# Kernel tuning notes

Measured on AMD Instinct MI355X. Metric: run time of the kernel, lower is better.

The kernel has to match this reference:

```python
import jax, jax.numpy as jnp
import numpy as np

DATA_NUM = 1024
CLS_NUM = 32000


def setup_inputs() -> dict:
    key = jax.random.key(0)
    k1, k2, k3, k4 = jax.random.split(key, 4)
    h1 = jax.random.normal(k1, (DATA_NUM, 2), dtype=jnp.float32) + 3.0
    e1 = jax.random.normal(k2, (CLS_NUM, 2), dtype=jnp.float32)
    h3 = jax.random.normal(k3, (DATA_NUM, 2), dtype=jnp.float32) * 2.0
    e3 = jax.random.normal(k4, (CLS_NUM, 2), dtype=jnp.float32)
    return {"h1": h1, "e1": e1, "h3": h3, "e3": e3, "share_head": 0}


def cal_akl(l1, l2):
    # l1: student logits (D, C); l2: teacher logits (D, C)
    probs1 = jax.nn.softmax(l1, axis=-1)
    probs2 = jax.nn.softmax(l2, axis=-1)
    # sort teacher probs ascending; gather student probs in same order
    sorted_idx = jnp.argsort(probs2, axis=-1)
    sorted_probs2 = jnp.take_along_axis(probs2, sorted_idx, axis=-1)
    sorted_probs1 = jnp.take_along_axis(probs1, sorted_idx, axis=-1)
    gap = jnp.abs(sorted_probs2 - sorted_probs1)
    cum_probs2 = jnp.cumsum(sorted_probs2, axis=-1)
    tail_mask = (cum_probs2 < 0.5).astype(l1.dtype)
    g_head = jax.lax.stop_gradient(jnp.sum(gap * (1.0 - tail_mask), axis=-1))
    g_tail = jax.lax.stop_gradient(jnp.sum(gap * tail_mask, axis=-1))
    lprobs1 = jax.nn.log_softmax(l1, axis=-1)
    lprobs2 = jax.nn.log_softmax(l2, axis=-1)
    fkl = jnp.sum(probs2 * (lprobs2 - lprobs1), axis=-1)
    rkl = jnp.sum(probs1 * (lprobs1 - lprobs2), axis=-1)
    denom = g_head + g_tail
    akl = (g_head / denom) * fkl + (g_tail / denom) * rkl
    return jnp.mean(akl)


def reference(h1, e1, h3, e3, share_head):
    # share_head is a static Python int/bool; obj == 'akl', share_head == 0 path
    if share_head:
        raise NotImplementedError("reference covers share_head=False path")
    stu_logits = h1 @ e1.T   # (D, C)
    tea_logits = h3 @ e3.T   # (D, C)
    return cal_akl(stu_logits, tea_logits)
```

## Files before the change

### kernel.cpp

```cpp
#include <hip/hip_runtime.h>
#include <math.h>

#define DNUM 1024
#define CNUM 32000
#define NT 512
#define R 2
#define GRID (DNUM / R)
#define KC 4
#define KF 8
#define NQ (CNUM / 4)
#define NFULL (NQ / NT)
#define TAILN (NQ - NFULL*NT)

#define L2E 1.4426950408889634f
#define LN2 0.6931471805599453f

typedef float v2f __attribute__((ext_vector_type(2)));

__device__ __forceinline__ v2f splat2(float s) { v2f v; v.x = s; v.y = s; return v; }

__device__ __forceinline__ float wave_red_sum(float v) {
    #pragma unroll
    for (int o = 32; o > 0; o >>= 1) v += __shfl_down(v, o, 64);
    return v;
}

__global__ __launch_bounds__(NT, 4) void akl_rows(
    const float* __restrict__ h1, const float* __restrict__ e1,
    const float* __restrict__ h3, const float* __restrict__ e3,
    float* __restrict__ out)
{
    const int tid  = threadIdx.x;
    const int lane = tid & 63, wid = tid >> 6;
    const int row0 = blockIdx.x * R;

    __shared__ float pool[16384];
    __shared__ float red[48];
    __shared__ float shCS[R*KC];
    __shared__ float shFP[R*KF], shFG[R*KF];
    __shared__ float shA[R][7];

    float a1L[R], b1L[R], a2L[R], b2L[R], mh1L[R], mh2L[R], icwC[R], c0C[R];
    #pragma unroll
    for (int r = 0; r < R; r++) {
        a1L[r] = h1[2*(row0+r)] * L2E; b1L[r] = h1[2*(row0+r)+1] * L2E;
        a2L[r] = h3[2*(row0+r)] * L2E; b2L[r] = h3[2*(row0+r)+1] * L2E;
        mh1L[r] = 6.0f * (fabsf(a1L[r]) + fabsf(b1L[r]));
        mh2L[r] = 6.0f * (fabsf(a2L[r]) + fabsf(b2L[r]));
        float sp = fmaxf(sqrtf(a2L[r]*a2L[r] + b2L[r]*b2L[r]), 1e-6f);
        icwC[r] = 1.0f / (1.35f * sp);
        c0C[r] = 0.5f/1.35f + mh2L[r]*icwC[r];
    }
    for (int i = tid; i < 16384; i += NT) pool[i] = 0.f;
    __syncthreads();

    const float4* __restrict__ E1 = (const float4*)e1;
    const float4* __restrict__ E3 = (const float4*)e3;

    const int cnt = NFULL + ((tid < TAILN) ? 1 : 0);

    v2f U1v[R], S1v[R], S2v[R];
    #pragma unroll
    for (int r = 0; r < R; r++) { U1v[r] = splat2(0.f); S1v[r] = splat2(0.f); S2v[r] = splat2(0.f); }

    auto body1 = [&](float4 A0, float4 A1, float4 B0, float4 B1) {
        #pragma unroll
        for (int r = 0; r < R; r++) {
            const v2f a1v = splat2(a1L[r]), b1v = splat2(b1L[r]);
            const v2f a2v = splat2(a2L[r]), b2v = splat2(b2L[r]);
            const v2f m1v = splat2(-mh1L[r]), m2v = splat2(-mh2L[r]);
            const v2f icv = splat2(icwC[r]), c0v = splat2(c0C[r]);
            #pragma unroll
            for (int p = 0; p < 2; p++) {
                float4 A = p ? A1 : A0, B = p ? B1 : B0;
                v2f X1; X1.x = A.x; X1.y = A.z;
                v2f Y1; Y1.x = A.y; Y1.y = A.w;
                v2f X3; X3.x = B.x; X3.y = B.z;
                v2f Y3; Y3.x = B.y; Y3.y = B.w;
                v2f l1 = a1v*X1 + (b1v*Y1 + m1v);
                v2f l2 = a2v*X3 + (b2v*Y3 + m2v);
                v2f e1v; e1v.x = __builtin_amdgcn_exp2f(l1.x);
                         e1v.y = __builtin_amdgcn_exp2f(l1.y);
                v2f e2v; e2v.x = __builtin_amdgcn_exp2f(l2.x);
                         e2v.y = __builtin_amdgcn_exp2f(l2.y);
                v2f dp = l2 - l1;
                U1v[r] += e1v;
                S1v[r] += e1v * dp;
                S2v[r] += e2v * dp;
                v2f t = l2*icv + c0v;
                float t0 = fminf(fmaxf(t.x, 0.f), 3.f);
                float t1 = fminf(fmaxf(t.y, 0.f), 3.f);
                int b0 = (int)t0, b1i = (int)t1;
                float* H0 = pool + (r*4 + 2*p    )*2048;
                float* H1 = pool + (r*4 + 2*p + 1)*2048;
                H0[b0*NT + tid]  += e2v.x;
                H1[b1i*NT + tid] += e2v.y;
            }
        }
    };

    {
        float4 cA0 = E1[2*tid], cA1 = E1[2*tid+1];
        float4 cB0 = E3[2*tid], cB1 = E3[2*tid+1];
        #pragma unroll 1
        for (int it = 0; it < cnt; ++it) {
            const int jn = (it+1 < cnt) ? ((it+1)*NT + tid) : tid;
            float4 nA0 = E1[2*jn], nA1 = E1[2*jn+1];
            float4 nB0 = E3[2*jn], nB1 = E3[2*jn+1];
            body1(cA0, cA1, cB0, cB1);
            cA0 = nA0; cA1 = nA1; cB0 = nB0; cB1 = nB1;
        }
    }

    #pragma unroll
    for (int r = 0; r < R; r++) {
        float u = wave_red_sum(U1v[r].x + U1v[r].y);
        float s1 = wave_red_sum(S1v[r].x + S1v[r].y);
        float s2 = wave_red_sum(S2v[r].x + S2v[r].y);
        if (lane == 0) {
            red[wid*6 + r*3 + 0] = u;
            red[wid*6 + r*3 + 1] = s1;
            red[wid*6 + r*3 + 2] = s2;
        }
    }
    __syncthreads();

    {
        int grp = tid >> 6, l = tid & 63;
        int r = grp >> 2, b = grp & 3;
        float s = 0.f;
        #pragma unroll
        for (int c = 0; c < 4; c++) {
            const float* H = pool + (r*4 + c)*2048 + b*512;
            #pragma unroll
            for (int t = 0; t < 8; t++) s += H[l + t*64];
        }
        s = wave_red_sum(s);
        if (l == 0) shCS[grp] = s;
    }
    __syncthreads();

    if (tid < R) {
        const int r = tid;
        float U1s = 0, S1s = 0, S2s = 0;
        for (int w = 0; w < 8; w++) {
            U1s += red[w*6 + r*3 + 0];
            S1s += red[w*6 + r*3 + 1];
            S2s += red[w*6 + r*3 + 2];
        }
        float U2s = 0.f;
        #pragma unroll
        for (int i = 0; i < KC; i++) U2s += shCS[r*KC + i];
        float mh1r = r ? mh1L[1] : mh1L[0];
        float mh2r = r ? mh2L[1] : mh2L[0];
        float a2r = r ? a2L[1] : a2L[0];
        float b2r = r ? b2L[1] : b2L[0];
        float dmh = mh2r - mh1r;
        S1s += dmh * U1s;
        S2s += dmh * U2s;
        float M1 = mh1r + __builtin_amdgcn_logf(U1s);
        float M2 = mh2r + __builtin_amdgcn_logf(U2s);
        float delta = M2 - M1;
        float thr = 0.5f * U2s;
        float S = 0.f; int bsel = KC-1;
        for (int i = 0; i < KC; i++) {
            float m = shCS[r*KC + i];
            if (S + m >= thr) { bsel = i; break; }
            S += m;
        }
        float sp = fmaxf(sqrtf(a2r*a2r + b2r*b2r), 1e-6f);
        float wc  = 1.35f * sp;
        float loS_s = fmaf((float)bsel, wc, -0.5f*sp) - mh2r;
        float icwF = (float)KF / wc;
        shA[r][0] = U2s / U1s;
        shA[r][1] = thr;
        shA[r][2] = LN2 * (S2s/U2s - delta);
        shA[r][3] = LN2 * (delta - S1s/U1s);
        shA[r][4] = icwF;
        shA[r][5] = -loS_s * icwF;
        shA[r][6] = S;
    }
    for (int i = tid; i < 16384; i += NT) pool[i] = 0.f;
    __syncthreads();

    float cR[R], icwFl[R], c0Fl[R];
    #pragma unroll
    for (int r = 0; r < R; r++) {
        cR[r] = shA[r][0]; icwFl[r] = shA[r][4]; c0Fl[r] = shA[r][5];
    }
    v2f gtv[R], Gpv[R];
    #pragma unroll
    for (int r = 0; r < R; r++) { gtv[r] = splat2(0.f); Gpv[r] = splat2(0.f); }

    auto body2 = [&](float4 A0, float4 A1, float4 B0, float4 B1) {
        #pragma unroll
        for (int r = 0; r < R; r++) {
            const v2f a1v = splat2(a1L[r]), b1v = splat2(b1L[r]);
            const v2f a2v = splat2(a2L[r]), b2v = splat2(b2L[r]);
            const v2f m1v = splat2(-mh1L[r]), m2v = splat2(-mh2L[r]);
            const v2f cv = splat2(-cR[r]);
            const v2f icv = splat2(icwFl[r]), c0v = splat2(c0Fl[r]);
            float* HP = pool + r*4096;
            float* HG = pool + (2+r)*4096;
            #pragma unroll
            for (int p = 0; p < 2; p++) {
                float4 A = p ? A1 : A0, B = p ? B1 : B0;
                v2f X1; X1.x = A.x; X1.y = A.z;
                v2f Y1; Y1.x = A.y; Y1.y = A.w;
                v2f X3; X3.x = B.x; X3.y = B.z;
                v2f Y3; Y3.x = B.y; Y3.y = B.w;
                v2f l1 = a1v*X1 + (b1v*Y1 + m1v);
                v2f l2 = a2v*X3 + (b2v*Y3 + m2v);
                v2f e1v; e1v.x = __builtin_amdgcn_exp2f(l1.x);
                         e1v.y = __builtin_amdgcn_exp2f(l1.y);
                v2f e2v; e2v.x = __builtin_amdgcn_exp2f(l2.x);
                         e2v.y = __builtin_amdgcn_exp2f(l2.y);
                v2f d = cv*e1v + e2v;
                v2f gap; gap.x = fabsf(d.x); gap.y = fabsf(d.y);
                gtv[r] += gap;
                v2f t = l2*icv + c0v;
                Gpv[r].x += (t.x < 0.f) ? gap.x : 0.f;
                Gpv[r].y += (t.y < 0.f) ? gap.y : 0.f;
                if (t.x >= 0.f && t.x < (float)KF) {
                    int fb = (int)t.x;
                    HP[fb*NT + tid] += e2v.x;
                    HG[fb*NT + tid] += gap.x;
                }
                if (t.y >= 0.f && t.y < (float)KF) {
                    int fb = (int)t.y;
                    HP[fb*NT + tid] += e2v.y;
                    HG[fb*NT + tid] += gap.y;
                }
            }
        }
    };

    {
        float4 cA0 = E1[2*tid], cA1 = E1[2*tid+1];
        float4 cB0 = E3[2*tid], cB1 = E3[2*tid+1];
        #pragma unroll 1
        for (int it = 0; it < cnt; ++it) {
            const int jn = (it+1 < cnt) ? ((it+1)*NT + tid) : tid;
            float4 nA0 = E1[2*jn], nA1 = E1[2*jn+1];
            float4 nB0 = E3[2*jn], nB1 = E3[2*jn+1];
            body2(cA0, cA1, cB0, cB1);
            cA0 = nA0; cA1 = nA1; cB0 = nB0; cB1 = nB1;
        }
    }

    #pragma unroll
    for (int r = 0; r < R; r++) {
        float a = wave_red_sum(gtv[r].x + gtv[r].y);
        float b = wave_red_sum(Gpv[r].x + Gpv[r].y);
        if (lane == 0) { red[wid*4 + r*2 + 0] = a; red[wid*4 + r*2 + 1] = b; }
    }
    __syncthreads();

    {
        int grp = tid >> 4, l16 = tid & 15;
        int isG = grp >> 4;
        int r = (grp >> 3) & 1, b = grp & 7;
        const float* H = pool + (isG*2 + r)*4096 + b*512;
        float s = 0.f;
        #pragma unroll
        for (int t = 0; t < NT/16; t++) s += H[l16 + t*16];
        #pragma unroll
        for (int o = 8; o > 0; o >>= 1) s += __shfl_down(s, o, 64);
        if (l16 == 0) {
            if (isG) shFG[r*KF + b] = s; else shFP[r*KF + b] = s;
        }
    }
    __syncthreads();

    if (tid < R) {
        const int r = tid;
        float gts = 0, Gp = 0;
        for (int w = 0; w < 8; w++) {
            gts += red[w*4 + r*2 + 0];
            Gp  += red[w*4 + r*2 + 1];
        }
        float thr = shA[r][1], fkl = shA[r][2], rkl = shA[r][3];
        float S = shA[r][6], G = Gp;
        bool done = false;
        #pragma unroll
        for (int i = 0; i < KF; i++) {
            if (!done) {
                float p = shFP[r*KF + i], g = shFG[r*KF + i];
                float ns = S + p;
                if (ns >= thr) {
                    float f = (thr - S) / fmaxf(p, 1e-30f);
                    f = fminf(fmaxf(f, 0.f), 1.f);
                    G += f * g;
                    done = true;
                } else { S = ns; G += g; }
            }
        }
        float gl = G;
        float gh = gts - gl;
        float akl = (gh*fkl + gl*rkl) / gts;
        unsafeAtomicAdd(out, akl * (1.0f/(float)DNUM));
    }
}

extern "C" void kernel_launch(void* const* d_in, const int* in_sizes, int n_in,
                              void* d_out, int out_size, void* d_ws, size_t ws_size,
                              hipStream_t stream) {
    const float* h1 = (const float*)d_in[0];
    const float* e1 = (const float*)d_in[1];
    const float* h3 = (const float*)d_in[2];
    const float* e3 = (const float*)d_in[3];
    hipMemsetAsync(d_out, 0, sizeof(float), stream);
    akl_rows<<<GRID, NT, 0, stream>>>(h1, e1, h3, e3, (float*)d_out);
}
```

Before: 106.2 us.

## Replace first-pass LDS histogram with register power-moment accumulators

The first pass no longer scatters teacher exp values into a 4-bin shared-memory histogram. Each thread keeps register sums of e, e*b, e*b^2 and e*b^3, where b is the integer bin index 0..3. The per-bin masses are then recovered by inverting the Vandermonde system on the reduced moments. This removes the initial pool zeroing, the LDS read-modify-writes, and one histogram reduction plus its barrier, at the cost of extra registers, more wave reductions, and possible float cancellation when recovering the bin masses.

Result: no change. 106.8 us, median of 3 (+0.6%).

```diff
diff --git a/kernel.cpp b/kernel.cpp
--- a/kernel.cpp
+++ b/kernel.cpp
@@ -35,8 +35,7 @@
     const int row0 = blockIdx.x * R;
 
     __shared__ float pool[16384];
-    __shared__ float red[48];
-    __shared__ float shCS[R*KC];
+    __shared__ float red[112];
     __shared__ float shFP[R*KF], shFG[R*KF];
     __shared__ float shA[R][7];
 
@@ -51,17 +50,19 @@
         icwC[r] = 1.0f / (1.35f * sp);
         c0C[r] = 0.5f/1.35f + mh2L[r]*icwC[r];
     }
-    for (int i = tid; i < 16384; i += NT) pool[i] = 0.f;
-    __syncthreads();
 
     const float4* __restrict__ E1 = (const float4*)e1;
     const float4* __restrict__ E3 = (const float4*)e3;
 
     const int cnt = NFULL + ((tid < TAILN) ? 1 : 0);
 
-    v2f U1v[R], S1v[R], S2v[R];
-    #pragma unroll
-    for (int r = 0; r < R; r++) { U1v[r] = splat2(0.f); S1v[r] = splat2(0.f); S2v[r] = splat2(0.f); }
+    v2f U1v[R], S1v[R], S2v[R], q0v[R], q1v[R], q2v[R], q3v[R];
+    #pragma unroll
+    for (int r = 0; r < R; r++) {
+        U1v[r] = splat2(0.f); S1v[r] = splat2(0.f); S2v[r] = splat2(0.f);
+        q0v[r] = splat2(0.f); q1v[r] = splat2(0.f);
+        q2v[r] = splat2(0.f); q3v[r] = splat2(0.f);
+    }
 
     auto body1 = [&](float4 A0, float4 A1, float4 B0, float4 B1) {
         #pragma unroll
@@ -88,13 +89,14 @@
                 S1v[r] += e1v * dp;
                 S2v[r] += e2v * dp;
                 v2f t = l2*icv + c0v;
-                float t0 = fminf(fmaxf(t.x, 0.f), 3.f);
-                float t1 = fminf(fmaxf(t.y, 0.f), 3.f);
-                int b0 = (int)t0, b1i = (int)t1;
-                float* H0 = pool + (r*4 + 2*p    )*2048;
-                float* H1 = pool + (r*4 + 2*p + 1)*2048;
-                H0[b0*NT + tid]  += e2v.x;
-                H1[b1i*NT + tid] += e2v.y;
+                v2f bfv;
+                bfv.x = truncf(fminf(fmaxf(t.x, 0.f), 3.f));
+                bfv.y = truncf(fminf(fmaxf(t.y, 0.f), 3.f));
+                v2f bf2 = bfv*bfv, bf3 = bf2*bfv;
+                q0v[r] += e2v;
+                q1v[r] += e2v * bfv;
+                q2v[r] += e2v * bf2;
+                q3v[r] += e2v * bf3;
             }
         }
     };
@@ -114,43 +116,45 @@
 
     #pragma unroll
     for (int r = 0; r < R; r++) {
-        float u = wave_red_sum(U1v[r].x + U1v[r].y);
-        float s1 = wave_red_sum(S1v[r].x + S1v[r].y);
-        float s2 = wave_red_sum(S2v[r].x + S2v[r].y);
+        float v0 = wave_red_sum(U1v[r].x + U1v[r].y);
+        float v1 = wave_red_sum(S1v[r].x + S1v[r].y);
+        float v2 = wave_red_sum(S2v[r].x + S2v[r].y);
+        float v3 = wave_red_sum(q0v[r].x + q0v[r].y);
+        float v4 = wave_red_sum(q1v[r].x + q1v[r].y);
+        float v5 = wave_red_sum(q2v[r].x + q2v[r].y);
+        float v6 = wave_red_sum(q3v[r].x + q3v[r].y);
         if (lane == 0) {
-            red[wid*6 + r*3 + 0] = u;
-            red[wid*6 + r*3 + 1] = s1;
-            red[wid*6 + r*3 + 2] = s2;
-        }
-    }
-    __syncthreads();
-
+            red[wid*14 + r*7 + 0] = v0; red[wid*14 + r*7 + 1] = v1;
+            red[wid*14 + r*7 + 2] = v2; red[wid*14 + r*7 + 3] = v3;
+            red[wid*14 + r*7 + 4] = v4; red[wid*14 + r*7 + 5] = v5;
+            red[wid*14 + r*7 + 6] = v6;
+        }
+    }
     {
-        int grp = tid >> 6, l = tid & 63;
-        int r = grp >> 2, b = grp & 3;
-        float s = 0.f;
-        #pragma unroll
-        for (int c = 0; c < 4; c++) {
-            const float* H = pool + (r*4 + c)*2048 + b*512;
-            #pragma unroll
-            for (int t = 0; t < 8; t++) s += H[l + t*64];
-        }
-        s = wave_red_sum(s);
-        if (l == 0) shCS[grp] = s;
+        float4* P4 = reinterpret_cast<float4*>(pool);
+        float4 z; z.x = 0.f; z.y = 0.f; z.z = 0.f; z.w = 0.f;
+        for (int i = tid; i < 4096; i += NT) P4[i] = z;
     }
     __syncthreads();
 
     if (tid < R) {
         const int r = tid;
-        float U1s = 0, S1s = 0, S2s = 0;
+        float U1s = 0, S1s = 0, S2s = 0, Q0 = 0, Q1 = 0, Q2 = 0, Q3 = 0;
         for (int w = 0; w < 8; w++) {
-            U1s += red[w*6 + r*3 + 0];
-            S1s += red[w*6 + r*3 + 1];
-            S2s += red[w*6 + r*3 + 2];
-        }
-        float U2s = 0.f;
-        #pragma unroll
-        for (int i = 0; i < KC; i++) U2s += shCS[r*KC + i];
+            U1s += red[w*14 + r*7 + 0];
+            S1s += red[w*14 + r*7 + 1];
+            S2s += red[w*14 + r*7 + 2];
+            Q0  += red[w*14 + r*7 + 3];
+            Q1  += red[w*14 + r*7 + 4];
+            Q2  += red[w*14 + r*7 + 5];
+            Q3  += red[w*14 + r*7 + 6];
+        }
+        float U2s = Q0;
+        float sb[KC];
+        sb[0] = Q0 - (11.f*Q1 - 6.f*Q2 + Q3) * (1.f/6.f);
+        sb[1] = (6.f*Q1 - 5.f*Q2 + Q3) * 0.5f;
+        sb[2] = (4.f*Q2 - 3.f*Q1 - Q3) * 0.5f;
+        sb[3] = (2.f*Q1 - 3.f*Q2 + Q3) * (1.f/6.f);
         float mh1r = r ? mh1L[1] : mh1L[0];
         float mh2r = r ? mh2L[1] : mh2L[0];
         float a2r = r ? a2L[1] : a2L[0];
@@ -163,8 +167,9 @@
         float delta = M2 - M1;
         float thr = 0.5f * U2s;
         float S = 0.f; int bsel = KC-1;
+        #pragma unroll
         for (int i = 0; i < KC; i++) {
-            float m = shCS[r*KC + i];
+            float m = sb[i];
             if (S + m >= thr) { bsel = i; break; }
             S += m;
         }
@@ -180,7 +185,6 @@
         shA[r][5] = -loS_s * icwF;
         shA[r][6] = S;
     }
-    for (int i = tid; i < 16384; i += NT) pool[i] = 0.f;
     __syncthreads();
 
     float cR[R], icwFl[R], c0Fl[R];
```
